# Performance work log

Hardware: AMD Instinct MI355X
Metric: run time of the kernel (lower is better)

Reference implementation:

```python
import jax, jax.numpy as jnp
import numpy as np

EMBED_DIM = 1024
NUM_HEADS = 16
NUM_GLOBAL = 4
NUM_LOCAL = NUM_HEADS - NUM_GLOBAL
WINDOW = 256
HEAD_DIM = EMBED_DIM // NUM_HEADS


def setup_inputs() -> dict:
    key = jax.random.key(0)
    k1, k2, k3 = jax.random.split(key, 3)
    B, S = 4, 2048
    x = jax.random.normal(k1, (B, S, EMBED_DIM), dtype=jnp.float32)
    w_qkv = jax.random.normal(k2, (EMBED_DIM, 3 * EMBED_DIM), dtype=jnp.float32) * (EMBED_DIM ** -0.5)
    b_qkv = jnp.zeros((3 * EMBED_DIM,), dtype=jnp.float32)
    w_out = jax.random.normal(k3, (EMBED_DIM, EMBED_DIM), dtype=jnp.float32) * (EMBED_DIM ** -0.5)
    b_out = jnp.zeros((EMBED_DIM,), dtype=jnp.float32)
    return {"x": x, "w_qkv": w_qkv, "b_qkv": b_qkv, "w_out": w_out, "b_out": b_out}


def _masks(seq_len):
    i = jnp.arange(seq_len)[:, None]
    j = jnp.arange(seq_len)[None, :]
    diff = i - j
    global_mask = diff < 0                      # True = masked (strictly future)
    local_mask = (diff < 0) | (diff > WINDOW)   # True = masked (outside window)
    return global_mask, local_mask


def _attend(q, k, v, mask):
    # q,k,v: [B,h,S,D]; mask: [S,S] True = disallow
    scores = jnp.einsum('bhqd,bhkd->bhqk', q, k) * (HEAD_DIM ** -0.5)
    scores = jnp.where(mask[None, None], -jnp.inf, scores)
    w = jax.nn.softmax(scores, axis=-1)
    return jnp.einsum('bhqk,bhkd->bhqd', w, v)


def reference(x, w_qkv, b_qkv, w_out, b_out):
    B, S, _ = x.shape
    qkv = x @ w_qkv + b_qkv                      # [B,S,3E]
    q, k, v = jnp.split(qkv, 3, axis=-1)
    def heads(t):
        return t.reshape(B, S, NUM_HEADS, HEAD_DIM).transpose(0, 2, 1, 3)
    q, k, v = heads(q), heads(k), heads(v)       # [B,H,S,D]
    gmask, lmask = _masks(S)
    ctx_g = _attend(q[:, :NUM_GLOBAL], k[:, :NUM_GLOBAL], v[:, :NUM_GLOBAL], gmask)
    ctx_l = _attend(q[:, NUM_GLOBAL:], k[:, NUM_GLOBAL:], v[:, NUM_GLOBAL:], lmask)
    ctx = jnp.concatenate([ctx_g, ctx_l], axis=1)          # [B,H,S,D]
    ctx = ctx.transpose(0, 2, 1, 3).reshape(B, S, EMBED_DIM)
    return ctx @ w_out + b_out
```

## Files before the change

kernel.cpp:

```cpp
#include <hip/hip_runtime.h>
#include <stdint.h>

#define EMB 1024
#define SEQ 2048
#define NB 4
#define NH 16
#define HD 64
#define NGLOB 4
#define WIN 256
#define MTOT (NB*SEQ)
#define NQKV (3*EMB)

#define PART_U16 2176

typedef __attribute__((ext_vector_type(8))) short bf16x8;
typedef __attribute__((ext_vector_type(4))) float f32x4;
typedef __attribute__((ext_vector_type(16))) float f32x16;
typedef unsigned short u16;
typedef unsigned int u32;

__device__ __forceinline__ u16 f2bf(float f) {
  u32 u = __builtin_bit_cast(u32, f);
  u += 0x7fffu + ((u >> 16) & 1u);
  return (u16)(u >> 16);
}

__device__ __forceinline__ float bf2f(u16 v) {
  u32 u = (u32)v << 16;
  return __builtin_bit_cast(float, u);
}

__device__ __forceinline__ u32 pack2bf(float a, float b) {
  return (u32)f2bf(a) | ((u32)f2bf(b) << 16);
}

#define MFMA16(a, b, c) __builtin_amdgcn_mfma_f32_16x16x32_bf16(a, b, c, 0, 0, 0)
#define MFMA32(a, b, c) __builtin_amdgcn_mfma_f32_32x32x16_bf16(a, b, c, 0, 0, 0)
#define GLD16(g, l) __builtin_amdgcn_global_load_lds( \
    (const __attribute__((address_space(1))) void*)(g), \
    (__attribute__((address_space(3))) void*)(l), 16, 0, 0)

__global__ void k_cast(const float* __restrict__ in, u16* __restrict__ out, int n4) {
  int i = blockIdx.x * blockDim.x + threadIdx.x;
  if (i >= n4) return;
  float4 f = ((const float4*)in)[i];
  ushort4 o;
  o.x = f2bf(f.x); o.y = f2bf(f.y); o.z = f2bf(f.z); o.w = f2bf(f.w);
  ((ushort4*)out)[i] = o;
}

__global__ void k_transpose_cast(const float* __restrict__ w, u16* __restrict__ wt,
                                 int R, int C) {
  __shared__ float tile[32][33];
  int c0 = blockIdx.x * 32, r0 = blockIdx.y * 32;
  int tx = threadIdx.x, ty = threadIdx.y;
  #pragma unroll
  for (int j = 0; j < 32; j += 8)
    tile[ty + j][tx] = w[(size_t)(r0 + ty + j) * C + (c0 + tx)];
  __syncthreads();
  #pragma unroll
  for (int j = 0; j < 32; j += 8)
    wt[(size_t)(c0 + ty + j) * R + (r0 + tx)] = f2bf(tile[tx][ty + j]);
}

template <int EPI>
__global__ __launch_bounds__(256, 2) void k_gemm(
    const u16* __restrict__ A, const u16* __restrict__ Bt,
    const float* __restrict__ bias,
    u16* __restrict__ Qo, u16* __restrict__ Ko, u16* __restrict__ Vt,
    float* __restrict__ outp) {
  __shared__ __align__(16) u16 ldsA[128 * 64];
  __shared__ __align__(16) u16 ldsB[128 * 64];
  const int tid = threadIdx.x;
  const int w = tid >> 6, lane = tid & 63;
  const int wm = w >> 1, wn = w & 1;
  const int m0 = blockIdx.x * 128, n0 = blockIdx.y * 128;
  const int rq = lane & 15, g = lane >> 4;

  const int srow = lane >> 3;
  const int scol = ((lane & 7) ^ srow) << 3;

  f32x4 acc[4][4] = {};
  char* ldsAb = (char*)ldsA;
  char* ldsBb = (char*)ldsB;

  for (int k0 = 0; k0 < EMB; k0 += 64) {
    #pragma unroll
    for (int it = 0; it < 4; ++it) {
      int t = w * 4 + it;
      int row = t * 8 + srow;
      GLD16(A + (size_t)(m0 + row) * EMB + k0 + scol, ldsAb + t * 1024);
      GLD16(Bt + (size_t)(n0 + row) * EMB + k0 + scol, ldsBb + t * 1024);
    }
    __syncthreads();
    #pragma unroll
    for (int ks = 0; ks < 2; ++ks) {
      bf16x8 af[4], bfr[4];
      #pragma unroll
      for (int i = 0; i < 4; ++i) {
        int rowA = wm * 64 + i * 16 + rq;
        int off = (ks * 64 + (g << 4)) ^ ((rowA & 7) << 4);
        af[i] = *(const bf16x8*)(ldsAb + rowA * 128 + off);
        int rowB = wn * 64 + i * 16 + rq;
        int offb = (ks * 64 + (g << 4)) ^ ((rowB & 7) << 4);
        bfr[i] = *(const bf16x8*)(ldsBb + rowB * 128 + offb);
      }
      #pragma unroll
      for (int mi = 0; mi < 4; ++mi)
        #pragma unroll
        for (int ni = 0; ni < 4; ++ni)
          acc[mi][ni] = MFMA16(af[mi], bfr[ni], acc[mi][ni]);
    }
    __syncthreads();
  }

  #pragma unroll
  for (int ni = 0; ni < 4; ++ni) {
    int col = n0 + wn * 64 + ni * 16 + rq;
    float bv = bias[col];
    if (EPI == 0) {
      int part = col >> 10;
      int hh = (col & 1023) >> 6;
      int d = col & 63;
      #pragma unroll
      for (int mi = 0; mi < 4; ++mi) {
        #pragma unroll
        for (int i = 0; i < 4; ++i) {
          int m = m0 + wm * 64 + mi * 16 + g * 4 + i;
          int b = m >> 11, s = m & 2047;
          u16 val = f2bf(acc[mi][ni][i] + bv);
          size_t bh = (size_t)(b * NH + hh);
          if (part == 0)      Qo[(bh * SEQ + s) * HD + d] = val;
          else if (part == 1) Ko[(bh * SEQ + s) * HD + d] = val;
          else                Vt[(bh * HD + d) * SEQ + s] = val;
        }
      }
    } else {
      #pragma unroll
      for (int mi = 0; mi < 4; ++mi)
        #pragma unroll
        for (int i = 0; i < 4; ++i) {
          int m = m0 + wm * 64 + mi * 16 + g * 4 + i;
          outp[(size_t)m * EMB + col] = acc[mi][ni][i] + bv;
        }
    }
  }
}

__global__ __launch_bounds__(256, 4) void k_attn(
    const u16* __restrict__ Q, const u16* __restrict__ K,
    const u16* __restrict__ Vt, u16* __restrict__ ctx,
    u16* __restrict__ part) {
  const int w = threadIdx.x >> 6, lane = threadIdx.x & 63;
  const int l31 = lane & 31;
  const int hi = lane >> 5;
  const bool hib = hi != 0;
  const int hi8 = hi * 8, hi4 = hi * 4;

  const int gid = blockIdx.x;
  const bool isglob = gid < 1024;

  int bh, qt, cstart, clen;
  if (isglob) {
    int bg = gid & 15;
    int j = gid >> 4;
    qt = ((j & 3) << 4) | (j >> 2);
    bh = (bg >> 2) * 16 + (bg & 3);
    int L = qt + 1;
    int base = L >> 2, rem = L & 3;
    clen = base + (w < rem ? 1 : 0);
    cstart = w * base + (w < rem ? w : rem);
  } else {
    int lidx = (gid - 1024) * 4 + w;
    int bl = lidx >> 6;
    bh = (bl / 12) * 16 + 4 + (bl % 12);
    qt = lidx & 63;
    int qb_ = qt * 32;
    int klo = (qb_ > WIN) ? qb_ - WIN : 0;
    cstart = klo >> 5;
    clen = qt + 1 - cstart;
  }

  const int qb = qt * 32;
  const int h = bh & 15;
  const int b = bh >> 4;
  const bool isloc = !isglob;

  const u16* Qp = Q + (size_t)bh * SEQ * HD;
  const u16* Kp = K + (size_t)bh * SEQ * HD;
  const u16* Vp = Vt + (size_t)bh * HD * SEQ;

  const int q = qb + l31;

  bf16x8 qf[4];
  #pragma unroll
  for (int j = 0; j < 4; ++j)
    qf[j] = *(const bf16x8*)(Qp + (size_t)q * HD + j * 16 + hi8);

  f32x16 oacc[2] = {};
  float m = -__builtin_inff();
  float l = 0.f;

  int kc = cstart * 32;
  for (int it = 0; it < clen; ++it, kc += 32) {
    f32x16 s = {};
    #pragma unroll
    for (int j = 0; j < 4; ++j) {
      bf16x8 kf = *(const bf16x8*)(Kp + (size_t)(kc + l31) * HD + j * 16 + hi8);
      s = MFMA32(kf, qf[j], s);
    }

    float p[16];
    float cmax = -__builtin_inff();
    #pragma unroll
    for (int r = 0; r < 16; ++r) {
      int key = kc + hi4 + (r & 3) + 8 * (r >> 2);
      float v = s[r] * 0.125f;
      bool msk = (key > q) || (isloc && (q - key > WIN));
      p[r] = msk ? -__builtin_inff() : v;
      cmax = fmaxf(cmax, p[r]);
    }
    cmax = fmaxf(cmax, __shfl_xor(cmax, 32));

    float mu;
    if (__any(cmax > m + 8.f)) {
      float mn = fmaxf(m, cmax);
      mu = (mn == -__builtin_inff()) ? 0.f : mn;
      float f = __expf(((m == -__builtin_inff()) ? mu : m) - mu);
      m = mn;
      l *= f;
      #pragma unroll
      for (int dt = 0; dt < 2; ++dt)
        #pragma unroll
        for (int r = 0; r < 16; ++r)
          oacc[dt][r] *= f;
    } else {
      mu = (m == -__builtin_inff()) ? 0.f : m;
    }

    float psum = 0.f;
    #pragma unroll
    for (int r = 0; r < 16; ++r) {
      p[r] = __expf(p[r] - mu);
      psum += p[r];
    }
    psum += __shfl_xor(psum, 32);
    l += psum;

    union { u32 u[4]; bf16x8 v; } pbf[2];
    #pragma unroll
    for (int sl = 0; sl < 2; ++sl) {
      int s8 = sl * 8;
      u32 X0 = pack2bf(p[s8 + 0], p[s8 + 1]);
      u32 X1 = pack2bf(p[s8 + 2], p[s8 + 3]);
      u32 X2 = pack2bf(p[s8 + 4], p[s8 + 5]);
      u32 X3 = pack2bf(p[s8 + 6], p[s8 + 7]);
      u32 oX0 = (u32)__shfl_xor((int)X0, 32);
      u32 oX1 = (u32)__shfl_xor((int)X1, 32);
      u32 oX2 = (u32)__shfl_xor((int)X2, 32);
      u32 oX3 = (u32)__shfl_xor((int)X3, 32);
      pbf[sl].u[0] = hib ? oX2 : X0;
      pbf[sl].u[1] = hib ? oX3 : X1;
      pbf[sl].u[2] = hib ? X2 : oX0;
      pbf[sl].u[3] = hib ? X3 : oX1;
    }

    #pragma unroll
    for (int dt = 0; dt < 2; ++dt) {
      #pragma unroll
      for (int sl = 0; sl < 2; ++sl) {
        bf16x8 vf = *(const bf16x8*)(Vp + (size_t)(dt * 32 + l31) * SEQ + kc + sl * 16 + hi8);
        oacc[dt] = MFMA32(vf, pbf[sl].v, oacc[dt]);
      }
    }
  }

  if (isglob) {
    u16* PB = part + (size_t)(gid * 4 + w) * PART_U16;
    #pragma unroll
    for (int dt = 0; dt < 2; ++dt)
      #pragma unroll
      for (int r = 0; r < 16; ++r) {
        int d = dt * 32 + hi4 + (r & 3) + 8 * (r >> 2);
        PB[d * 32 + l31] = f2bf(oacc[dt][r]);
      }
    float* PF = (float*)(PB + 2048);
    if (hi == 0) { PF[l31] = m; PF[32 + l31] = l; }
  } else {
    float linv = 1.f / l;
    #pragma unroll
    for (int dt = 0; dt < 2; ++dt) {
      #pragma unroll
      for (int r = 0; r < 16; ++r) {
        int d = dt * 32 + hi4 + (r & 3) + 8 * (r >> 2);
        int e = h * HD + d;
        ctx[(size_t)(b * SEQ + q) * EMB + e] = f2bf(oacc[dt][r] * linv);
      }
    }
  }
}

__global__ __launch_bounds__(256, 4) void k_merge(
    const u16* __restrict__ part, u16* __restrict__ ctx) {
  const int t = blockIdx.x;
  const int bg = t & 15;
  const int j = t >> 4;
  const int qt = ((j & 3) << 4) | (j >> 2);
  const int bh = (bg >> 2) * 16 + (bg & 3);
  const int qb = qt * 32;
  const int h = bh & 15;
  const int b = bh >> 4;

  const u16* P0 = part + (size_t)(t * 4 + 0) * PART_U16;
  const u16* P1 = part + (size_t)(t * 4 + 1) * PART_U16;
  const u16* P2 = part + (size_t)(t * 4 + 2) * PART_U16;
  const u16* P3 = part + (size_t)(t * 4 + 3) * PART_U16;
  const float* F0 = (const float*)(P0 + 2048);
  const float* F1 = (const float*)(P1 + 2048);
  const float* F2 = (const float*)(P2 + 2048);
  const float* F3 = (const float*)(P3 + 2048);

  const int tid = threadIdx.x;
  const int dd = tid & 63;
  const int qg = tid >> 6;
  #pragma unroll
  for (int i = 0; i < 8; ++i) {
    int qq = qg * 8 + i;
    float m0v = F0[qq], m1v = F1[qq], m2v = F2[qq], m3v = F3[qq];
    float M = fmaxf(fmaxf(m0v, m1v), fmaxf(m2v, m3v));
    float w0 = __expf(m0v - M), w1 = __expf(m1v - M);
    float w2 = __expf(m2v - M), w3 = __expf(m3v - M);
    float L = w0 * F0[32 + qq] + w1 * F1[32 + qq] +
              w2 * F2[32 + qq] + w3 * F3[32 + qq];
    float val = w0 * bf2f(P0[dd * 32 + qq]) + w1 * bf2f(P1[dd * 32 + qq]) +
                w2 * bf2f(P2[dd * 32 + qq]) + w3 * bf2f(P3[dd * 32 + qq]);
    int s = qb + qq;
    ctx[(size_t)(b * SEQ + s) * EMB + h * HD + dd] = f2bf(val / L);
  }
}

extern "C" void kernel_launch(void* const* d_in, const int* in_sizes, int n_in,
                              void* d_out, int out_size, void* d_ws, size_t ws_size,
                              hipStream_t stream) {
  const float* x     = (const float*)d_in[0];
  const float* w_qkv = (const float*)d_in[1];
  const float* b_qkv = (const float*)d_in[2];
  const float* w_out = (const float*)d_in[3];
  const float* b_out = (const float*)d_in[4];
  float* out = (float*)d_out;

  char* ws = (char*)d_ws;
  u16* xb    = (u16*)(ws);
  u16* wqkvT = (u16*)(ws + (16ull << 20));
  u16* woutT = (u16*)(ws + (22ull << 20));
  u16* Qb    = (u16*)(ws + (24ull << 20));
  u16* Kb    = (u16*)(ws + (40ull << 20));
  u16* Vt    = (u16*)(ws + (56ull << 20));
  u16* ctx   = (u16*)(ws + (72ull << 20));
  u16* part  = xb;

  k_cast<<<(MTOT * EMB / 4) / 256, 256, 0, stream>>>(x, xb, MTOT * EMB / 4);
  dim3 tb(32, 8);
  k_transpose_cast<<<dim3(NQKV / 32, EMB / 32), tb, 0, stream>>>(w_qkv, wqkvT, EMB, NQKV);
  k_transpose_cast<<<dim3(EMB / 32, EMB / 32), tb, 0, stream>>>(w_out, woutT, EMB, EMB);

  k_gemm<0><<<dim3(MTOT / 128, NQKV / 128), 256, 0, stream>>>(
      xb, wqkvT, b_qkv, Qb, Kb, Vt, nullptr);

  k_attn<<<dim3(1024 + 768), 256, 0, stream>>>(Qb, Kb, Vt, ctx, part);
  k_merge<<<dim3(1024), 256, 0, stream>>>(part, ctx);

  k_gemm<1><<<dim3(MTOT / 128, EMB / 128), 256, 0, stream>>>(
      ctx, woutT, b_out, nullptr, nullptr, nullptr, out);
}
```

Measured before the change: 205.0 us.

## Streamline attention inner loop with exp2, split MFMA chains, and conditional masking

Folds the 1/sqrt(d) scale into the exp2 argument (fma with log2e/8) instead of scaling every score, uses the hardware exp2 builtin, and splits the QK dot product into two independent MFMA accumulation chains. Per-element masking now runs only on diagonal or window-edge tiles, bf16 packing of probabilities truncates instead of rounding, and the loop is unrolled by two. The merge kernel rescales stored unscaled maxima by 0.125 to match. Truncation adds a small downward bias in P, and the rescale threshold is adjusted for unscaled scores.

```diff
diff --git a/kernel.cpp b/kernel.cpp
--- a/kernel.cpp
+++ b/kernel.cpp
@@ -19,6 +19,14 @@
 typedef unsigned short u16;
 typedef unsigned int u32;
 
+#define CL2 0.18033688011112042f
+
+#if __has_builtin(__builtin_amdgcn_exp2f)
+#define EXP2(x) __builtin_amdgcn_exp2f(x)
+#else
+#define EXP2(x) exp2f(x)
+#endif
+
 __device__ __forceinline__ u16 f2bf(float f) {
   u32 u = __builtin_bit_cast(u32, f);
   u += 0x7fffu + ((u >> 16) & 1u);
@@ -30,8 +38,10 @@
   return __builtin_bit_cast(float, u);
 }
 
-__device__ __forceinline__ u32 pack2bf(float a, float b) {
-  return (u32)f2bf(a) | ((u32)f2bf(b) << 16);
+__device__ __forceinline__ u32 packtrunc(float a, float b) {
+  u32 ua = __builtin_bit_cast(u32, a);
+  u32 ub = __builtin_bit_cast(u32, b);
+  return (ua >> 16) | (ub & 0xffff0000u);
 }
 
 #define MFMA16(a, b, c) __builtin_amdgcn_mfma_f32_16x16x32_bf16(a, b, c, 0, 0, 0)
@@ -191,6 +201,7 @@
   const u16* Vp = Vt + (size_t)bh * HD * SEQ;
 
   const int q = qb + l31;
+  const float NINF = -__builtin_inff();
 
   bf16x8 qf[4];
   #pragma unroll
@@ -198,35 +209,51 @@
     qf[j] = *(const bf16x8*)(Qp + (size_t)q * HD + j * 16 + hi8);
 
   f32x16 oacc[2] = {};
-  float m = -__builtin_inff();
+  float m = NINF;
   float l = 0.f;
 
   int kc = cstart * 32;
+  #pragma unroll 2
   for (int it = 0; it < clen; ++it, kc += 32) {
-    f32x16 s = {};
-    #pragma unroll
-    for (int j = 0; j < 4; ++j) {
-      bf16x8 kf = *(const bf16x8*)(Kp + (size_t)(kc + l31) * HD + j * 16 + hi8);
-      s = MFMA32(kf, qf[j], s);
-    }
-
+    f32x16 s0 = {}, s1 = {};
+    {
+      bf16x8 kf0 = *(const bf16x8*)(Kp + (size_t)(kc + l31) * HD + 0 + hi8);
+      bf16x8 kf1 = *(const bf16x8*)(Kp + (size_t)(kc + l31) * HD + 16 + hi8);
+      bf16x8 kf2 = *(const bf16x8*)(Kp + (size_t)(kc + l31) * HD + 32 + hi8);
+      bf16x8 kf3 = *(const bf16x8*)(Kp + (size_t)(kc + l31) * HD + 48 + hi8);
+      s0 = MFMA32(kf0, qf[0], s0);
+      s1 = MFMA32(kf2, qf[2], s1);
+      s0 = MFMA32(kf1, qf[1], s0);
+      s1 = MFMA32(kf3, qf[3], s1);
+    }
+
+    const bool needs_mask = (kc == qb) || (isloc && (qb - kc > 225));
     float p[16];
-    float cmax = -__builtin_inff();
-    #pragma unroll
-    for (int r = 0; r < 16; ++r) {
-      int key = kc + hi4 + (r & 3) + 8 * (r >> 2);
-      float v = s[r] * 0.125f;
-      bool msk = (key > q) || (isloc && (q - key > WIN));
-      p[r] = msk ? -__builtin_inff() : v;
-      cmax = fmaxf(cmax, p[r]);
+    float cmax = NINF;
+    if (needs_mask) {
+      #pragma unroll
+      for (int r = 0; r < 16; ++r) {
+        int key = kc + hi4 + (r & 3) + 8 * (r >> 2);
+        float v = s0[r] + s1[r];
+        bool bad = (key > q) || (isloc && (q - key > WIN));
+        p[r] = bad ? NINF : v;
+        cmax = fmaxf(cmax, p[r]);
+      }
+    } else {
+      #pragma unroll
+      for (int r = 0; r < 16; ++r) {
+        p[r] = s0[r] + s1[r];
+        cmax = fmaxf(cmax, p[r]);
+      }
     }
     cmax = fmaxf(cmax, __shfl_xor(cmax, 32));
 
-    float mu;
-    if (__any(cmax > m + 8.f)) {
+    float muC;
+    if (__any(cmax > m + 64.f)) {
       float mn = fmaxf(m, cmax);
-      mu = (mn == -__builtin_inff()) ? 0.f : mn;
-      float f = __expf(((m == -__builtin_inff()) ? mu : m) - mu);
+      muC = (mn == NINF) ? 0.f : mn * CL2;
+      float oldC = (m == NINF) ? muC : m * CL2;
+      float f = EXP2(oldC - muC);
       m = mn;
       l *= f;
       #pragma unroll
@@ -235,14 +262,15 @@
         for (int r = 0; r < 16; ++r)
           oacc[dt][r] *= f;
     } else {
-      mu = (m == -__builtin_inff()) ? 0.f : m;
+      muC = (m == NINF) ? 0.f : m * CL2;
     }
 
     float psum = 0.f;
     #pragma unroll
     for (int r = 0; r < 16; ++r) {
-      p[r] = __expf(p[r] - mu);
-      psum += p[r];
+      float e = EXP2(__builtin_fmaf(p[r], CL2, -muC));
+      p[r] = e;
+      psum += e;
     }
     psum += __shfl_xor(psum, 32);
     l += psum;
@@ -251,10 +279,10 @@
     #pragma unroll
     for (int sl = 0; sl < 2; ++sl) {
       int s8 = sl * 8;
-      u32 X0 = pack2bf(p[s8 + 0], p[s8 + 1]);
-      u32 X1 = pack2bf(p[s8 + 2], p[s8 + 3]);
-      u32 X2 = pack2bf(p[s8 + 4], p[s8 + 5]);
-      u32 X3 = pack2bf(p[s8 + 6], p[s8 + 7]);
+      u32 X0 = packtrunc(p[s8 + 0], p[s8 + 1]);
+      u32 X1 = packtrunc(p[s8 + 2], p[s8 + 3]);
+      u32 X2 = packtrunc(p[s8 + 4], p[s8 + 5]);
+      u32 X3 = packtrunc(p[s8 + 6], p[s8 + 7]);
       u32 oX0 = (u32)__shfl_xor((int)X0, 32);
       u32 oX1 = (u32)__shfl_xor((int)X1, 32);
       u32 oX2 = (u32)__shfl_xor((int)X2, 32);
@@ -328,8 +356,8 @@
     int qq = qg * 8 + i;
     float m0v = F0[qq], m1v = F1[qq], m2v = F2[qq], m3v = F3[qq];
     float M = fmaxf(fmaxf(m0v, m1v), fmaxf(m2v, m3v));
-    float w0 = __expf(m0v - M), w1 = __expf(m1v - M);
-    float w2 = __expf(m2v - M), w3 = __expf(m3v - M);
+    float w0 = __expf((m0v - M) * 0.125f), w1 = __expf((m1v - M) * 0.125f);
+    float w2 = __expf((m2v - M) * 0.125f), w3 = __expf((m3v - M) * 0.125f);
     float L = w0 * F0[32 + qq] + w1 * F1[32 + qq] +
               w2 * F2[32 + qq] + w3 * F3[32 + qq];
     float val = w0 * bf2f(P0[dd * 32 + qq]) + w1 * bf2f(P1[dd * 32 + qq]) +
```

New measurement: 204.0 us. No clear change (-0.5%).
